# Performance work log

Measured on AMD Instinct MI355X. Metric: run time of the kernel, lower is better.

Reference implementation:

```python
import jax, jax.numpy as jnp
import numpy as np
import math

SEQ = 2048
D = 1024
H = 16
DK = D // H  # 64
EPS = 1e-5


def setup_inputs() -> dict:
    key = jax.random.key(0)
    ks = jax.random.split(key, 10)
    s = 1.0 / math.sqrt(D)
    return {
        "x": jax.random.normal(ks[0], (SEQ, D), dtype=jnp.float32),
        "Wq": jax.random.uniform(ks[1], (D, D), jnp.float32, -s, s),
        "bq": jax.random.uniform(ks[2], (D,), jnp.float32, -s, s),
        "Wk": jax.random.uniform(ks[3], (D, D), jnp.float32, -s, s),
        "bk": jax.random.uniform(ks[4], (D,), jnp.float32, -s, s),
        "Wv": jax.random.uniform(ks[5], (D, D), jnp.float32, -s, s),
        "bv": jax.random.uniform(ks[6], (D,), jnp.float32, -s, s),
        "Wo": jax.random.uniform(ks[7], (D, D), jnp.float32, -s, s),
        "bo": jax.random.uniform(ks[8], (D,), jnp.float32, -s, s),
        "gamma": jnp.ones((D,), jnp.float32),
        "beta": jnp.zeros((D,), jnp.float32),
    }


def reference(x, Wq, bq, Wk, bk, Wv, bv, Wo, bo, gamma, beta):
    N = x.shape[0]
    # projections (Linear: x @ W + b)
    Q = (x @ Wq + bq).reshape(N, H, DK).transpose(1, 0, 2)  # [H,N,DK]
    K = (x @ Wk + bk).reshape(N, H, DK).transpose(1, 0, 2)
    V = (x @ Wv + bv).reshape(N, H, DK).transpose(1, 0, 2)
    # causal scores; mask applied before scaling as in original (-inf unaffected)
    scores = jnp.einsum("hqd,hkd->hqk", Q, K)  # [H,N,N]
    causal = jnp.tril(jnp.ones((N, N), dtype=bool))
    scores = jnp.where(causal[None], scores, -jnp.inf) / math.sqrt(DK)
    attn = jax.nn.softmax(scores, axis=-1)
    ctx = jnp.einsum("hqk,hkd->hqd", attn, V)  # [H,N,DK]
    ctx = ctx.transpose(1, 0, 2).reshape(N, D)  # concat heads
    y = ctx @ Wo + bo + x  # residual
    # LayerNorm over last dim
    mu = jnp.mean(y, axis=-1, keepdims=True)
    var = jnp.var(y, axis=-1, keepdims=True)
    return (y - mu) * jax.lax.rsqrt(var + EPS) * gamma + beta
```

## Files before the change

### kernel.cpp

```cpp
#include <hip/hip_runtime.h>
#include <hip/hip_bf16.h>

#define SEQ 2048
#define DMODEL 1024
#define NHEAD 16
#define DKH 64
#define NSPLIT 4

typedef __hip_bfloat16 bf16;
typedef __attribute__((ext_vector_type(8))) short short8;
typedef __attribute__((ext_vector_type(4))) float f32x4;

__device__ __forceinline__ unsigned short f2bf_bits(float f) {
    bf16 h = __float2bfloat16(f);
    return *reinterpret_cast<unsigned short*>(&h);
}

__device__ __forceinline__ unsigned pack_bf2(float a, float b) {
    return (unsigned)f2bf_bits(a) | ((unsigned)f2bf_bits(b) << 16);
}

__device__ __forceinline__ float bf_to_f(unsigned short u) {
    unsigned v = (unsigned)u << 16;
    return *(float*)&v;
}

__global__ __launch_bounds__(256) void cast_x_kernel(const float* __restrict__ x,
                                                     bf16* __restrict__ xb) {
    int i = (blockIdx.x * 256 + threadIdx.x) * 4;
    float4 v = *(const float4*)(x + i);
    ushort4 o;
    o.x = f2bf_bits(v.x); o.y = f2bf_bits(v.y);
    o.z = f2bf_bits(v.z); o.w = f2bf_bits(v.w);
    *(ushort4*)(xb + i) = o;
}

__global__ __launch_bounds__(256) void transpose_cast_w4(const float* __restrict__ W0,
                                                         const float* __restrict__ W1,
                                                         const float* __restrict__ W2,
                                                         const float* __restrict__ W3,
                                                         bf16* __restrict__ Wqkv,
                                                         bf16* __restrict__ Wot) {
    const float* W = (blockIdx.z == 0) ? W0 : (blockIdx.z == 1) ? W1 : (blockIdx.z == 2) ? W2 : W3;
    bf16* out = (blockIdx.z < 3) ? (Wqkv + (size_t)blockIdx.z * DMODEL * DMODEL) : Wot;
    __shared__ float tile[32][33];
    int bx = blockIdx.x * 32;
    int by = blockIdx.y * 32;
    int tx = threadIdx.x;
    int ty = threadIdx.y;
    for (int i = 0; i < 32; i += 8)
        tile[ty + i][tx] = W[(by + ty + i) * DMODEL + bx + tx];
    __syncthreads();
    for (int i = 0; i < 32; i += 8)
        out[(bx + ty + i) * DMODEL + by + tx] = __float2bfloat16(tile[tx][ty + i]);
}

template <int FUSED>
__global__ __launch_bounds__(256) void gemm128(const bf16* __restrict__ A,
                                               const bf16* __restrict__ Bt,
                                               const float* __restrict__ b0,
                                               const float* __restrict__ b1,
                                               const float* __restrict__ b2,
                                               bf16* __restrict__ Qb,
                                               bf16* __restrict__ Kb,
                                               bf16* __restrict__ Vtb,
                                               const float* __restrict__ resid,
                                               float* __restrict__ yout) {
    const int m0 = blockIdx.y * 128;
    const int n0 = blockIdx.x * 64;
    __shared__ __align__(16) bf16 As[2][128 * 64];
    __shared__ __align__(16) bf16 Bs[2][64 * 64];
    const int tid = threadIdx.x, lane = tid & 63, wid = tid >> 6;
    const int l16 = lane & 15, lhi = lane >> 4;
    const int wr = wid >> 1, wc = wid & 1;

    f32x4 acc[4][2];
    for (int i = 0; i < 4; ++i)
        for (int j = 0; j < 2; ++j) acc[i][j] = (f32x4){0.f, 0.f, 0.f, 0.f};

    auto stage = [&](int kt, int buf) {
        #pragma unroll
        for (int j = 0; j < 6; ++j) {
            const int chunk = j * 256 + tid;
            if (j < 4) {
                const int row = chunk >> 3, c16 = chunk & 7;
                const bf16* gA = A + (size_t)(m0 + row) * DMODEL + kt + c16 * 8;
                __builtin_amdgcn_global_load_lds((const __attribute__((address_space(1))) void*)gA,
                                                 (__attribute__((address_space(3))) void*)(&As[buf][chunk * 8]),
                                                 16, 0, 0);
            } else {
                const int bc = chunk - 1024;
                const int row = bc >> 3, c16 = bc & 7;
                const bf16* gB = Bt + (size_t)(n0 + row) * DMODEL + kt + c16 * 8;
                __builtin_amdgcn_global_load_lds((const __attribute__((address_space(1))) void*)gB,
                                                 (__attribute__((address_space(3))) void*)(&Bs[buf][bc * 8]),
                                                 16, 0, 0);
            }
        }
    };

    stage(0, 0);

    int buf = 0;
    for (int t = 0; t < DMODEL / 64; ++t) {
        const bool pre = (t + 1 < DMODEL / 64);
        if (pre) {
            stage((t + 1) * 64, buf ^ 1);
            asm volatile("s_waitcnt vmcnt(6)" ::: "memory");
        } else {
            asm volatile("s_waitcnt vmcnt(0)" ::: "memory");
        }
        __builtin_amdgcn_s_barrier();
        __builtin_amdgcn_sched_barrier(0);
        #pragma unroll
        for (int c = 0; c < 2; ++c) {
            short8 af[4], bfm[2];
            #pragma unroll
            for (int mi = 0; mi < 4; ++mi)
                af[mi] = *(const short8*)(&As[buf][(wr * 64 + mi * 16 + l16) * 64 + c * 32 + lhi * 8]);
            #pragma unroll
            for (int ni = 0; ni < 2; ++ni)
                bfm[ni] = *(const short8*)(&Bs[buf][(wc * 32 + ni * 16 + l16) * 64 + c * 32 + lhi * 8]);
            #pragma unroll
            for (int mi = 0; mi < 4; ++mi)
                #pragma unroll
                for (int ni = 0; ni < 2; ++ni)
                    acc[mi][ni] = __builtin_amdgcn_mfma_f32_16x16x32_bf16(af[mi], bfm[ni], acc[mi][ni], 0, 0, 0);
        }
        __builtin_amdgcn_s_barrier();
        __builtin_amdgcn_sched_barrier(0);
        buf ^= 1;
    }

    if (FUSED) {
        const int reg = n0 >> 10;
        const float* bias = (reg == 0) ? b0 : (reg == 1) ? b1 : b2;
        const int nb = n0 & 1023;
        #pragma unroll
        for (int mi = 0; mi < 4; ++mi)
            #pragma unroll
            for (int ni = 0; ni < 2; ++ni) {
                const int gm = m0 + wr * 64 + mi * 16 + lhi * 4;
                const int gn = nb + wc * 32 + ni * 16 + l16;
                const float bv = bias[gn];
                if (reg == 0) {
                    for (int r = 0; r < 4; ++r)
                        Qb[(size_t)(gm + r) * DMODEL + gn] = __float2bfloat16((acc[mi][ni][r] + bv) * 0.125f);
                } else if (reg == 1) {
                    for (int r = 0; r < 4; ++r)
                        Kb[(size_t)(gm + r) * DMODEL + gn] = __float2bfloat16(acc[mi][ni][r] + bv);
                } else {
                    ushort4 p;
                    p.x = f2bf_bits(acc[mi][ni][0] + bv);
                    p.y = f2bf_bits(acc[mi][ni][1] + bv);
                    p.z = f2bf_bits(acc[mi][ni][2] + bv);
                    p.w = f2bf_bits(acc[mi][ni][3] + bv);
                    *(ushort4*)(&Vtb[(size_t)gn * SEQ + gm]) = p;
                }
            }
    } else {
        #pragma unroll
        for (int mi = 0; mi < 4; ++mi)
            #pragma unroll
            for (int ni = 0; ni < 2; ++ni) {
                const int gm = m0 + wr * 64 + mi * 16 + lhi * 4;
                const int gn = n0 + wc * 32 + ni * 16 + l16;
                const float bv = b0[gn];
                for (int r = 0; r < 4; ++r)
                    yout[(size_t)(gm + r) * DMODEL + gn] =
                        acc[mi][ni][r] + bv + resid[(size_t)(gm + r) * DMODEL + gn];
            }
    }
}

__global__ __launch_bounds__(256) void attn_kernel(const bf16* __restrict__ Q,
                                                   const bf16* __restrict__ K,
                                                   const bf16* __restrict__ Vt,
                                                   bf16* __restrict__ Opart,
                                                   float* __restrict__ Lpart) {
    const int s = blockIdx.y;
    const int h = blockIdx.x;
    const int qb = 15 - (s >> 2);
    const int sp = s & 3;

    const int tid = threadIdx.x;
    const int lane = tid & 63, w = tid >> 6;
    const int l16 = lane & 15, m = lane >> 4;
    const int q0w = qb * 128 + w * 32;

    __shared__ __align__(16) bf16 Ks[2][64 * 64];
    __shared__ __align__(16) bf16 Vs[2][64 * 64];

    short8 qf[2][2];
    #pragma unroll
    for (int g = 0; g < 2; ++g)
        #pragma unroll
        for (int c = 0; c < 2; ++c)
            qf[g][c] = *(const short8*)(&Q[(size_t)(q0w + g * 16 + l16) * DMODEL + h * DKH + c * 32 + m * 8]);

    f32x4 oacc[2][4];
    #pragma unroll
    for (int g = 0; g < 2; ++g)
        #pragma unroll
        for (int dn = 0; dn < 4; ++dn) oacc[g][dn] = (f32x4){0.f, 0.f, 0.f, 0.f};
    float lrp[2] = {0.f, 0.f};

    const int ntt = 2 * (qb + 1);
    const int lo = (ntt * sp) / NSPLIT;
    const int hi_t = (ntt * (sp + 1)) / NSPLIT;

    const int srcA = l16 + ((m & 1) << 5);
    const int srcB = srcA + 16;
    const bool hilane = (m >> 1) != 0;

    const int r0 = tid >> 3;
    const int cbyte = (tid & 7) * 16;
    auto stage = [&](int t, int buf) {
        #pragma unroll
        for (int j = 0; j < 2; ++j) {
            const int r = j * 32 + r0;
            const int sc = cbyte ^ ((r & 7) << 4);
            const bf16* gk = K + (size_t)(t * 64 + r) * DMODEL + h * DKH + (sc >> 1);
            const bf16* gv = Vt + (size_t)(h * DKH + r) * SEQ + t * 64 + (sc >> 1);
            __builtin_amdgcn_global_load_lds((const __attribute__((address_space(1))) void*)gk,
                                             (__attribute__((address_space(3))) void*)(&Ks[buf][j * 2048 + tid * 8]),
                                             16, 0, 0);
            __builtin_amdgcn_global_load_lds((const __attribute__((address_space(1))) void*)gv,
                                             (__attribute__((address_space(3))) void*)(&Vs[buf][j * 2048 + tid * 8]),
                                             16, 0, 0);
        }
    };

    if (lo < hi_t) {
        stage(lo, 0);

        const int rsw = (l16 & 7) << 3;

        for (int t = lo; t < hi_t; ++t) {
            const int cur = (t - lo) & 1;
            const bool pre = (t + 1 < hi_t);
            if (pre) {
                stage(t + 1, cur ^ 1);
                asm volatile("s_waitcnt vmcnt(4)" ::: "memory");
            } else {
                asm volatile("s_waitcnt vmcnt(0)" ::: "memory");
            }
            __builtin_amdgcn_s_barrier();
            __builtin_amdgcn_sched_barrier(0);
            const int k0 = t * 64;

            if (k0 <= q0w + 31) {
                const bool masked = (k0 + 63 > q0w);

                short8 kf[4][2], vf[4][2];
                #pragma unroll
                for (int n = 0; n < 4; ++n)
                    #pragma unroll
                    for (int c = 0; c < 2; ++c)
                        kf[n][c] = *(const short8*)(&Ks[cur][(n * 16 + l16) * 64 + ((c * 32 + m * 8) ^ rsw)]);
                #pragma unroll
                for (int dn = 0; dn < 4; ++dn)
                    #pragma unroll
                    for (int c = 0; c < 2; ++c)
                        vf[dn][c] = *(const short8*)(&Vs[cur][(dn * 16 + l16) * 64 + ((c * 32 + m * 8) ^ rsw)]);

                f32x4 sv[2][4];
                #pragma unroll
                for (int g = 0; g < 2; ++g)
                    #pragma unroll
                    for (int n = 0; n < 4; ++n) {
                        f32x4 a = (f32x4){0.f, 0.f, 0.f, 0.f};
                        a = __builtin_amdgcn_mfma_f32_16x16x32_bf16(kf[n][0], qf[g][0], a, 0, 0, 0);
                        a = __builtin_amdgcn_mfma_f32_16x16x32_bf16(kf[n][1], qf[g][1], a, 0, 0, 0);
                        sv[g][n] = a;
                    }

                unsigned pk01[2][4], pk23[2][4];
                #pragma unroll
                for (int g = 0; g < 2; ++g) {
                    const int q = q0w + g * 16 + l16;
                    float rsp = 0.f;
                    #pragma unroll
                    for (int n = 0; n < 4; ++n) {
                        float v0 = sv[g][n][0], v1 = sv[g][n][1], v2 = sv[g][n][2], v3 = sv[g][n][3];
                        if (masked) {
                            const int kb = k0 + n * 16 + m * 4;
                            if (kb + 0 > q) v0 = -1e30f;
                            if (kb + 1 > q) v1 = -1e30f;
                            if (kb + 2 > q) v2 = -1e30f;
                            if (kb + 3 > q) v3 = -1e30f;
                        }
                        float p0 = __expf(v0);
                        float p1 = __expf(v1);
                        float p2 = __expf(v2);
                        float p3 = __expf(v3);
                        rsp += (p0 + p1) + (p2 + p3);
                        pk01[g][n] = pack_bf2(p0, p1);
                        pk23[g][n] = pack_bf2(p2, p3);
                    }
                    lrp[g] += rsp;
                }

                #pragma unroll
                for (int g = 0; g < 2; ++g) {
                    union { short8 s8; unsigned u[4]; } bfr[2];
                    #pragma unroll
                    for (int cb = 0; cb < 2; ++cb) {
                        unsigned w0a = __shfl((int)pk01[g][2 * cb], srcA, 64);
                        unsigned w0b = __shfl((int)pk01[g][2 * cb + 1], srcA, 64);
                        unsigned w1a = __shfl((int)pk23[g][2 * cb], srcA, 64);
                        unsigned w1b = __shfl((int)pk23[g][2 * cb + 1], srcA, 64);
                        unsigned w2a = __shfl((int)pk01[g][2 * cb], srcB, 64);
                        unsigned w2b = __shfl((int)pk01[g][2 * cb + 1], srcB, 64);
                        unsigned w3a = __shfl((int)pk23[g][2 * cb], srcB, 64);
                        unsigned w3b = __shfl((int)pk23[g][2 * cb + 1], srcB, 64);
                        bfr[cb].u[0] = hilane ? w0b : w0a;
                        bfr[cb].u[1] = hilane ? w1b : w1a;
                        bfr[cb].u[2] = hilane ? w2b : w2a;
                        bfr[cb].u[3] = hilane ? w3b : w3a;
                    }
                    #pragma unroll
                    for (int dn = 0; dn < 4; ++dn) {
                        oacc[g][dn] = __builtin_amdgcn_mfma_f32_16x16x32_bf16(vf[dn][0], bfr[0].s8, oacc[g][dn], 0, 0, 0);
                        oacc[g][dn] = __builtin_amdgcn_mfma_f32_16x16x32_bf16(vf[dn][1], bfr[1].s8, oacc[g][dn], 0, 0, 0);
                    }
                }
            }
            __builtin_amdgcn_s_barrier();
            __builtin_amdgcn_sched_barrier(0);
        }
    }

    #pragma unroll
    for (int g = 0; g < 2; ++g) {
        float rs = lrp[g];
        rs += __shfl_xor(rs, 16, 64);
        rs += __shfl_xor(rs, 32, 64);
        const int q = q0w + g * 16 + l16;
        bf16* base = Opart + ((size_t)(h * SEQ + q) * NSPLIT + sp) * 64 + m * 4;
        #pragma unroll
        for (int dn = 0; dn < 4; ++dn) {
            unsigned a = pack_bf2(oacc[g][dn][0], oacc[g][dn][1]);
            unsigned b = pack_bf2(oacc[g][dn][2], oacc[g][dn][3]);
            *(unsigned*)(base + dn * 16) = a;
            *(unsigned*)(base + dn * 16 + 2) = b;
        }
        if (m == 0)
            Lpart[(size_t)(h * SEQ + q) * NSPLIT + sp] = rs;
    }
}

__global__ __launch_bounds__(256) void attn_combine(const bf16* __restrict__ Opart,
                                                    const float* __restrict__ Lpart,
                                                    bf16* __restrict__ ctx) {
    const int flat = blockIdx.x * 256 + threadIdx.x;
    const int d4 = flat & 15;
    const int q = (flat >> 4) & 2047;
    const int h = flat >> 15;
    const size_t pbase = (size_t)(h * SEQ + q) * NSPLIT;

    const float4 lv = *(const float4*)(&Lpart[pbase]);
    const float inv = 1.f / (lv.x + lv.y + lv.z + lv.w);

    float acc0 = 0.f, acc1 = 0.f, acc2 = 0.f, acc3 = 0.f;
    #pragma unroll
    for (int i = 0; i < NSPLIT; ++i) {
        const ushort4 o = *(const ushort4*)(&Opart[(pbase + i) * 64 + d4 * 4]);
        acc0 += bf_to_f(o.x);
        acc1 += bf_to_f(o.y);
        acc2 += bf_to_f(o.z);
        acc3 += bf_to_f(o.w);
    }
    ushort4 r;
    r.x = f2bf_bits(acc0 * inv);
    r.y = f2bf_bits(acc1 * inv);
    r.z = f2bf_bits(acc2 * inv);
    r.w = f2bf_bits(acc3 * inv);
    *(ushort4*)(&ctx[(size_t)q * DMODEL + h * DKH + d4 * 4]) = r;
}

__global__ __launch_bounds__(256) void ln_kernel(const float* __restrict__ y,
                                                 const float* __restrict__ gamma,
                                                 const float* __restrict__ beta,
                                                 float* __restrict__ out) {
    const int row = blockIdx.x;
    const int col = threadIdx.x * 4;
    float4 v = *(const float4*)(y + row * DMODEL + col);
    float s = v.x + v.y + v.z + v.w;
    float q = v.x * v.x + v.y * v.y + v.z * v.z + v.w * v.w;
    for (int off = 1; off < 64; off <<= 1) {
        s += __shfl_xor(s, off, 64);
        q += __shfl_xor(q, off, 64);
    }
    __shared__ float ss[4], sq[4];
    int wid = threadIdx.x >> 6;
    if ((threadIdx.x & 63) == 0) { ss[wid] = s; sq[wid] = q; }
    __syncthreads();
    s = ss[0] + ss[1] + ss[2] + ss[3];
    q = sq[0] + sq[1] + sq[2] + sq[3];
    float mu = s * (1.f / DMODEL);
    float var = q * (1.f / DMODEL) - mu * mu;
    float rstd = rsqrtf(var + 1e-5f);
    float4 g = *(const float4*)(gamma + col);
    float4 b = *(const float4*)(beta + col);
    float4 o;
    o.x = (v.x - mu) * rstd * g.x + b.x;
    o.y = (v.y - mu) * rstd * g.y + b.y;
    o.z = (v.z - mu) * rstd * g.z + b.z;
    o.w = (v.w - mu) * rstd * g.w + b.w;
    *(float4*)(out + row * DMODEL + col) = o;
}

extern "C" void kernel_launch(void* const* d_in, const int* in_sizes, int n_in,
                              void* d_out, int out_size, void* d_ws, size_t ws_size,
                              hipStream_t stream) {
    const float* x     = (const float*)d_in[0];
    const float* Wq    = (const float*)d_in[1];
    const float* bq    = (const float*)d_in[2];
    const float* Wk    = (const float*)d_in[3];
    const float* bk    = (const float*)d_in[4];
    const float* Wv    = (const float*)d_in[5];
    const float* bv    = (const float*)d_in[6];
    const float* Wo    = (const float*)d_in[7];
    const float* bo    = (const float*)d_in[8];
    const float* gamma = (const float*)d_in[9];
    const float* beta  = (const float*)d_in[10];
    float* out = (float*)d_out;

    const size_t MB = 1024 * 1024;
    char* w = (char*)d_ws;
    bf16* Wot  = (bf16*)w;            w += 2 * MB;
    bf16* Qb   = (bf16*)w;            w += 4 * MB;
    bf16* Kb   = (bf16*)w;            w += 4 * MB;
    bf16* Vtb  = (bf16*)w;            w += 4 * MB;
    bf16* ctxb = (bf16*)w;            w += 4 * MB;
    char* pool = w;
    bf16* xb   = (bf16*)pool;
    bf16* Wqt  = (bf16*)(pool + 4 * MB);
    float* yb  = (float*)(pool + 10 * MB);
    bf16* Opart  = (bf16*)pool;
    float* Lpart = (float*)(pool + 16 * MB);

    cast_x_kernel<<<SEQ * DMODEL / (256 * 4), 256, 0, stream>>>(x, xb);

    dim3 tgrid(DMODEL / 32, DMODEL / 32, 4), tblk(32, 8);
    transpose_cast_w4<<<tgrid, tblk, 0, stream>>>(Wq, Wk, Wv, Wo, Wqt, Wot);

    dim3 qkvgrid(3 * DMODEL / 64, SEQ / 128);
    gemm128<1><<<qkvgrid, 256, 0, stream>>>(xb, Wqt, bq, bk, bv, Qb, Kb, Vtb, nullptr, nullptr);

    dim3 agrid(NHEAD, 16 * NSPLIT);
    attn_kernel<<<agrid, 256, 0, stream>>>(Qb, Kb, Vtb, Opart, Lpart);

    attn_combine<<<NHEAD * SEQ * 16 / 256, 256, 0, stream>>>(Opart, Lpart, ctxb);

    dim3 ogrid(DMODEL / 64, SEQ / 128);
    gemm128<0><<<ogrid, 256, 0, stream>>>(ctxb, Wot, bo, nullptr, nullptr, nullptr, nullptr, nullptr, x, yb);

    ln_kernel<<<SEQ, 256, 0, stream>>>(yb, gamma, beta, out);
}
```

Before: 94.66 us.

## Triple-buffer attention K/V tiles, drop trailing barrier, add MFMA priority, fuse prep kernels

Folds the x-cast kernel into the weight transpose kernel as an extra grid slice, which removes one launch. In attention, K/V LDS staging moves from double to triple buffering so the trailing per-iteration barrier can be dropped, since the buffer being refilled is never the one just read. MFMA sections are wrapped in s_setprio to favour matrix issue across waves. The cost is more LDS per block (possible occupancy loss), and correctness depends on the three-buffer rotation covering the race the removed barrier used to guard.

```diff
diff --git a/kernel.cpp b/kernel.cpp
--- a/kernel.cpp
+++ b/kernel.cpp
@@ -25,22 +25,27 @@
     return *(float*)&v;
 }
 
-__global__ __launch_bounds__(256) void cast_x_kernel(const float* __restrict__ x,
-                                                     bf16* __restrict__ xb) {
-    int i = (blockIdx.x * 256 + threadIdx.x) * 4;
-    float4 v = *(const float4*)(x + i);
-    ushort4 o;
-    o.x = f2bf_bits(v.x); o.y = f2bf_bits(v.y);
-    o.z = f2bf_bits(v.z); o.w = f2bf_bits(v.w);
-    *(ushort4*)(xb + i) = o;
-}
-
-__global__ __launch_bounds__(256) void transpose_cast_w4(const float* __restrict__ W0,
-                                                         const float* __restrict__ W1,
-                                                         const float* __restrict__ W2,
-                                                         const float* __restrict__ W3,
-                                                         bf16* __restrict__ Wqkv,
-                                                         bf16* __restrict__ Wot) {
+__global__ __launch_bounds__(256) void prep_kernel(const float* __restrict__ x,
+                                                   const float* __restrict__ W0,
+                                                   const float* __restrict__ W1,
+                                                   const float* __restrict__ W2,
+                                                   const float* __restrict__ W3,
+                                                   bf16* __restrict__ xb,
+                                                   bf16* __restrict__ Wqkv,
+                                                   bf16* __restrict__ Wot) {
+    if (blockIdx.z == 4) {
+        const int bid = blockIdx.y * 32 + blockIdx.x;
+        const int tid = threadIdx.y * 32 + threadIdx.x;
+        const size_t i = ((size_t)bid * 256 + tid) * 8;
+        float4 a = *(const float4*)(x + i);
+        float4 b = *(const float4*)(x + i + 4);
+        ushort4 o1, o2;
+        o1.x = f2bf_bits(a.x); o1.y = f2bf_bits(a.y); o1.z = f2bf_bits(a.z); o1.w = f2bf_bits(a.w);
+        o2.x = f2bf_bits(b.x); o2.y = f2bf_bits(b.y); o2.z = f2bf_bits(b.z); o2.w = f2bf_bits(b.w);
+        *(ushort4*)(xb + i) = o1;
+        *(ushort4*)(xb + i + 4) = o2;
+        return;
+    }
     const float* W = (blockIdx.z == 0) ? W0 : (blockIdx.z == 1) ? W1 : (blockIdx.z == 2) ? W2 : W3;
     bf16* out = (blockIdx.z < 3) ? (Wqkv + (size_t)blockIdx.z * DMODEL * DMODEL) : Wot;
     __shared__ float tile[32][33];
@@ -188,8 +193,8 @@
     const int l16 = lane & 15, m = lane >> 4;
     const int q0w = qb * 128 + w * 32;
 
-    __shared__ __align__(16) bf16 Ks[2][64 * 64];
-    __shared__ __align__(16) bf16 Vs[2][64 * 64];
+    __shared__ __align__(16) bf16 Ks[3][64 * 64];
+    __shared__ __align__(16) bf16 Vs[3][64 * 64];
 
     short8 qf[2][2];
     #pragma unroll
@@ -235,12 +240,12 @@
         stage(lo, 0);
 
         const int rsw = (l16 & 7) << 3;
+        int cur = 0, nxt = 1;
 
         for (int t = lo; t < hi_t; ++t) {
-            const int cur = (t - lo) & 1;
             const bool pre = (t + 1 < hi_t);
             if (pre) {
-                stage(t + 1, cur ^ 1);
+                stage(t + 1, nxt);
                 asm volatile("s_waitcnt vmcnt(4)" ::: "memory");
             } else {
                 asm volatile("s_waitcnt vmcnt(0)" ::: "memory");
@@ -265,6 +270,7 @@
                         vf[dn][c] = *(const short8*)(&Vs[cur][(dn * 16 + l16) * 64 + ((c * 32 + m * 8) ^ rsw)]);
 
                 f32x4 sv[2][4];
+                __builtin_amdgcn_s_setprio(1);
                 #pragma unroll
                 for (int g = 0; g < 2; ++g)
                     #pragma unroll
@@ -274,6 +280,7 @@
                         a = __builtin_amdgcn_mfma_f32_16x16x32_bf16(kf[n][1], qf[g][1], a, 0, 0, 0);
                         sv[g][n] = a;
                     }
+                __builtin_amdgcn_s_setprio(0);
 
                 unsigned pk01[2][4], pk23[2][4];
                 #pragma unroll
@@ -319,15 +326,17 @@
                         bfr[cb].u[2] = hilane ? w2b : w2a;
                         bfr[cb].u[3] = hilane ? w3b : w3a;
                     }
+                    __builtin_amdgcn_s_setprio(1);
                     #pragma unroll
                     for (int dn = 0; dn < 4; ++dn) {
                         oacc[g][dn] = __builtin_amdgcn_mfma_f32_16x16x32_bf16(vf[dn][0], bfr[0].s8, oacc[g][dn], 0, 0, 0);
                         oacc[g][dn] = __builtin_amdgcn_mfma_f32_16x16x32_bf16(vf[dn][1], bfr[1].s8, oacc[g][dn], 0, 0, 0);
                     }
+                    __builtin_amdgcn_s_setprio(0);
                 }
             }
-            __builtin_amdgcn_s_barrier();
-            __builtin_amdgcn_sched_barrier(0);
+            cur = nxt;
+            nxt = (nxt + 1 == 3) ? 0 : nxt + 1;
         }
     }
 
@@ -441,10 +450,8 @@
     bf16* Opart  = (bf16*)pool;
     float* Lpart = (float*)(pool + 16 * MB);
 
-    cast_x_kernel<<<SEQ * DMODEL / (256 * 4), 256, 0, stream>>>(x, xb);
-
-    dim3 tgrid(DMODEL / 32, DMODEL / 32, 4), tblk(32, 8);
-    transpose_cast_w4<<<tgrid, tblk, 0, stream>>>(Wq, Wk, Wv, Wo, Wqt, Wot);
+    dim3 tgrid(DMODEL / 32, DMODEL / 32, 5), tblk(32, 8);
+    prep_kernel<<<tgrid, tblk, 0, stream>>>(x, Wq, Wk, Wv, Wo, xb, Wqt, Wot);
 
     dim3 qkvgrid(3 * DMODEL / 64, SEQ / 128);
     gemm128<1><<<qkvgrid, 256, 0, stream>>>(xb, Wqt, bq, bk, bv, Qb, Kb, Vtb, nullptr, nullptr);
```

Result: faster. 90.26 us (-4.6%).
